# Kernel optimization log

Hardware: AMD Instinct MI355X
Metric: run time of the kernel (lower is better)

The kernel has to match this reference:

```python
import jax, jax.numpy as jnp
import numpy as np

N = 3072      # num topics / nodes
D_IN = 64     # topic_dim
HID = 128     # hidden_dim
NH = 4        # n_heads
HD = HID // NH
L = 2         # n_gat_layers
B = 1024      # batch of topic_ids
ALPHA = 0.2   # leaky relu slope
TD = 0.1      # time decay
EPS = 1e-5    # layernorm eps


def setup_inputs() -> dict:
    key = jax.random.key(0)
    ks = jax.random.split(key, 16)
    rn = lambda k, s, sc=0.05: (jax.random.normal(k, s, jnp.float32) * sc)
    return {
        "topic_ids": jax.random.randint(ks[0], (B,), 0, N, dtype=jnp.int32),
        "adj_matrix": jax.random.randint(ks[1], (N, N), 0, 2).astype(jnp.float32),
        "time_matrix": jax.random.uniform(ks[2], (N, N), dtype=jnp.float32),
        "attractiveness": jax.random.normal(ks[3], (B,), jnp.float32),
        "topic_emb": rn(ks[4], (N, D_IN), 0.1),
        "Ws": rn(ks[5], (D_IN, HID)), "bs": jnp.zeros((HID,), jnp.float32),
        "Wa": rn(ks[6], (1, HID)), "ba": jnp.zeros((HID,), jnp.float32),
        "gat_W": rn(ks[7], (L, NH, HID, HD)),
        "gat_a": rn(ks[8], (L, NH, 2 * HD, 1)),
        "ln_g": jnp.ones((L, HID), jnp.float32),
        "ln_b": jnp.zeros((L, HID), jnp.float32),
        "W1": rn(ks[9], (HID, HID)), "b1": jnp.zeros((HID,), jnp.float32),
        "W2": rn(ks[10], (HID, 1)), "b2": jnp.zeros((1,), jnp.float32),
    }


def _gat_layer(x, adj, tmat, W, a, g, b):
    # x: [1, N, HID], adj/tmat: [N, N], W: [NH, HID, HD], a: [NH, 2*HD, 1]
    time_weights = jnp.exp(-TD * (tmat.max() - tmat))          # [N, N]
    h = jnp.einsum('bni,hio->bhno', x, W)                      # [1, NH, N, HD]
    a_src, a_dst = a[:, :HD, 0], a[:, HD:, 0]                  # [NH, HD]
    e_src = jnp.einsum('bhnd,hd->bhn', h, a_src)               # [1, NH, N]
    e_dst = jnp.einsum('bhnd,hd->bhn', h, a_dst)
    e = e_src[:, :, :, None] + e_dst[:, :, None, :]            # [1, NH, N, N]
    e = jax.nn.leaky_relu(e, ALPHA) * time_weights[None, None]
    mask = adj[None, None]                                     # [1, 1, N, N]
    e = jnp.where(mask == 0, -jnp.inf, e)
    has_nb = mask.sum(axis=-1) > 0                             # [1, 1, N]
    e = jnp.where(has_nb[..., None], e, 0.0)                   # isolated rows -> zeros -> uniform softmax (matches torch)
    att = jax.nn.softmax(e, axis=-1)
    att = jnp.where(jnp.isnan(att), 0.0, att)
    out = jnp.einsum('bhij,bhjo->bhio', att, h)                # [1, NH, N, HD]
    out = out.transpose(0, 2, 1, 3).reshape(1, N, NH * HD)
    out = jax.nn.elu(out)
    mu = out.mean(axis=-1, keepdims=True)
    var = out.var(axis=-1, keepdims=True)
    return (out - mu) / jnp.sqrt(var + EPS) * g + b


def reference(topic_ids, adj_matrix, time_matrix, attractiveness, topic_emb,
              Ws, bs, Wa, ba, gat_W, gat_a, ln_g, ln_b, W1, b1, W2, b2):
    struct = topic_emb @ Ws + bs                               # [N, HID]
    attract = attractiveness[:, None] @ Wa + ba                # [B, HID]
    x = struct[None]                                           # [1, N, HID]
    for l in range(L):
        x = _gat_layer(x, adj_matrix, time_matrix, gat_W[l], gat_a[l], ln_g[l], ln_b[l])
    topic_feats = x[0][topic_ids]                              # [B, HID]
    hidden = jax.nn.relu((topic_feats + attract) @ W1 + b1)
    return hidden @ W2 + b2                                    # [B, 1]
```

## Files before the change

kernel.cpp:

```cpp
#include <hip/hip_runtime.h>
#include <hip/hip_fp16.h>

#define N 3072
#define D_IN 64
#define HID 128
#define NH 4
#define HD 32
#define NB 1024
#define ALPHA 0.2f
#define TD 0.1f
#define EPS 1e-5f
#define LOG2E 1.4426950408889634f
#define TSPLIT 16
#define JSPAN (N / TSPLIT)
#define NCH (JSPAN / 64)
#define PSTR 72

typedef unsigned int uint;
typedef unsigned short ushort;
typedef __attribute__((ext_vector_type(8))) __bf16 bf16x8;
typedef __attribute__((ext_vector_type(4))) float f32x4;

__device__ __forceinline__ ushort f2bf(float f) {
  union { float f; uint u; } c; c.f = f;
  uint u = c.u;
  return (ushort)((u + 0x7FFFu + ((u >> 16) & 1u)) >> 16);
}

__global__ __launch_bounds__(256) void k_prep1(const float4* __restrict__ tmat4,
                                               uint* __restrict__ tmax_u) {
  int g = blockIdx.x * 256 + threadIdx.x;
  float mx = 0.f;
#pragma unroll
  for (int k = 0; k < 9; k++) {
    float4 v = tmat4[g + k * 262144];
    mx = fmaxf(mx, fmaxf(fmaxf(v.x, v.y), fmaxf(v.z, v.w)));
  }
  for (int o = 32; o > 0; o >>= 1) mx = fmaxf(mx, __shfl_xor(mx, o));
  __shared__ float sm[4];
  if ((threadIdx.x & 63) == 0) sm[threadIdx.x >> 6] = mx;
  __syncthreads();
  if (threadIdx.x == 0) {
    float m = fmaxf(fmaxf(sm[0], sm[1]), fmaxf(sm[2], sm[3]));
    atomicMax(tmax_u, __float_as_uint(m));
  }
}

__global__ __launch_bounds__(256) void k_prep2(const float* __restrict__ tmat,
                                               const float* __restrict__ adj,
                                               const uint* __restrict__ tmax_u,
                                               ushort* __restrict__ aw,
                                               uint* __restrict__ deg0) {
  int row = blockIdx.x * 4 + (threadIdx.x >> 6);
  int lane = threadIdx.x & 63;
  float tmax = __uint_as_float(*tmax_u);
  const float c1 = TD * LOG2E;
  const float4* tr = (const float4*)(tmat + (size_t)row * N);
  const float4* ar = (const float4*)(adj + (size_t)row * N);
  ushort* ao = aw + (size_t)row * N;
  float s = 0.f;
#pragma unroll
  for (int it = 0; it < 12; it++) {
    int c4 = lane + it * 64;
    float4 t4 = tr[c4];
    float4 a4 = ar[c4];
    s += a4.x + a4.y + a4.z + a4.w;
    float w0 = __builtin_amdgcn_exp2f(c1 * (t4.x - tmax)) * LOG2E;
    float w1 = __builtin_amdgcn_exp2f(c1 * (t4.y - tmax)) * LOG2E;
    float w2 = __builtin_amdgcn_exp2f(c1 * (t4.z - tmax)) * LOG2E;
    float w3 = __builtin_amdgcn_exp2f(c1 * (t4.w - tmax)) * LOG2E;
    ushort u0 = (a4.x != 0.f) ? __half_as_ushort(__float2half(w0)) : (ushort)0;
    ushort u1 = (a4.y != 0.f) ? __half_as_ushort(__float2half(w1)) : (ushort)0;
    ushort u2 = (a4.z != 0.f) ? __half_as_ushort(__float2half(w2)) : (ushort)0;
    ushort u3 = (a4.w != 0.f) ? __half_as_ushort(__float2half(w3)) : (ushort)0;
    uint2 pk;
    pk.x = (uint)u0 | ((uint)u1 << 16);
    pk.y = (uint)u2 | ((uint)u3 << 16);
    *(uint2*)(ao + c4 * 4) = pk;
  }
  for (int o = 32; o > 0; o >>= 1) s += __shfl_xor(s, o);
  if (lane == 0) deg0[row] = (s == 0.f) ? 1u : 0u;
}

__global__ __launch_bounds__(128) void k_struct(const float* __restrict__ emb,
                                                const float* __restrict__ Ws,
                                                const float* __restrict__ bs,
                                                float* __restrict__ x0) {
  int n = blockIdx.x, c = threadIdx.x;
  __shared__ float es_[D_IN];
  if (c < D_IN) es_[c] = emb[n * D_IN + c];
  __syncthreads();
  float acc = bs[c];
#pragma unroll
  for (int i = 0; i < D_IN; i++) acc += es_[i] * Ws[i * HID + c];
  x0[(size_t)n * HID + c] = acc;
}

__global__ __launch_bounds__(256) void k_h(const float* __restrict__ x,
                                           const float* __restrict__ gW,
                                           const float* __restrict__ gA,
                                           ushort* __restrict__ hT,
                                           float* __restrict__ es,
                                           float* __restrict__ ed) {
  int n0 = blockIdx.x * 8;
  int t = threadIdx.x;
  __shared__ float xs[8][HID];
  __shared__ float hs[8][HID];
  for (int k = t; k < 8 * HID; k += 256) xs[k >> 7][k & 127] = x[(size_t)n0 * HID + k];
  __syncthreads();
  int c = t & 127, rh = t >> 7;
  const float* Wc = gW + (c >> 5) * (HID * HD) + (c & 31);
  float acc[4] = {0.f, 0.f, 0.f, 0.f};
  for (int i = 0; i < HID; i++) {
    float wv = Wc[i * HD];
#pragma unroll
    for (int r4 = 0; r4 < 4; r4++) acc[r4] += xs[rh + 2 * r4][i] * wv;
  }
#pragma unroll
  for (int r4 = 0; r4 < 4; r4++) hs[rh + 2 * r4][c] = acc[r4];
  __syncthreads();
  if (t < 64) {
    int r = t >> 3, h_ = (t >> 1) & 3, sd = t & 1;
    const float* av = gA + h_ * (2 * HD) + sd * HD;
    float d = 0.f;
#pragma unroll
    for (int k = 0; k < HD; k++) d += hs[r][h_ * HD + k] * av[k];
    (sd ? ed : es)[h_ * N + n0 + r] = d;
  }
  {
    int half = t >> 7;
    ushort pk[4];
#pragma unroll
    for (int r = 0; r < 4; r++) pk[r] = f2bf(hs[half * 4 + r][c]);
    uint2 v;
    v.x = (uint)pk[0] | ((uint)pk[1] << 16);
    v.y = (uint)pk[2] | ((uint)pk[3] << 16);
    *(uint2*)(&hT[(size_t)c * N + n0 + half * 4]) = v;
  }
}

__global__ __launch_bounds__(256) void k_att(const ushort* __restrict__ aw,
                                             const ushort* __restrict__ hT,
                                             const float* __restrict__ es,
                                             const float* __restrict__ ed,
                                             const uint* __restrict__ deg0,
                                             float* __restrict__ o_part,
                                             float* __restrict__ s_part) {
  __shared__ __align__(16) ushort ps[2][NH][32][PSTR];
  int tid = threadIdx.x;
  int ib = blockIdx.x * 32;
  int sp = blockIdx.y;
  int jb0 = sp * JSPAN;

  int jl = tid & 31;
  int ig = tid >> 5;
  float esr[4][NH];
  uint dg[4];
#pragma unroll
  for (int p = 0; p < 4; p++) {
    int i = ib + ig + 8 * p;
    dg[p] = deg0[i];
#pragma unroll
    for (int h_ = 0; h_ < NH; h_++) esr[p][h_] = es[h_ * N + i];
  }

  int wv = tid >> 6;
  int ln = tid & 63;
  f32x4 acc00 = {0.f, 0.f, 0.f, 0.f}, acc01 = {0.f, 0.f, 0.f, 0.f};
  f32x4 acc10 = {0.f, 0.f, 0.f, 0.f}, acc11 = {0.f, 0.f, 0.f, 0.f};
  float sacc[4][NH];
#pragma unroll
  for (int p = 0; p < 4; p++)
#pragma unroll
    for (int h_ = 0; h_ < NH; h_++) sacc[p][h_] = 0.f;

  uint awv[4];
  float2 edv[NH];

  auto LOADS = [&](int ch) {
    int j0 = jb0 + ch * 64 + 2 * jl;
#pragma unroll
    for (int p = 0; p < 4; p++)
      awv[p] = *(const uint*)&aw[(size_t)(ib + ig + 8 * p) * N + j0];
#pragma unroll
    for (int h_ = 0; h_ < NH; h_++) edv[h_] = *(const float2*)&ed[h_ * N + j0];
  };
  auto COMPUTE = [&](int buf) {
#pragma unroll
    for (int p = 0; p < 4; p++) {
      float a0 = __half2float(__ushort_as_half((ushort)(awv[p] & 0xFFFFu)));
      float a1 = __half2float(__ushort_as_half((ushort)(awv[p] >> 16)));
#pragma unroll
      for (int h_ = 0; h_ < NH; h_++) {
        float e0 = esr[p][h_] + edv[h_].x;
        float e1 = esr[p][h_] + edv[h_].y;
        float l0 = fmaxf(e0, 0.f) + ALPHA * fminf(e0, 0.f);
        float l1 = fmaxf(e1, 0.f) + ALPHA * fminf(e1, 0.f);
        float p0 = __builtin_amdgcn_exp2f(l0 * a0);
        float p1 = __builtin_amdgcn_exp2f(l1 * a1);
        p0 = (a0 != 0.f) ? p0 : 0.f;
        p1 = (a1 != 0.f) ? p1 : 0.f;
        if (dg[p]) { p0 = 1.f; p1 = 1.f; }
        sacc[p][h_] += p0 + p1;
        uint pk = (__float_as_uint(p0) >> 16) | (__float_as_uint(p1) & 0xFFFF0000u);
        *(uint*)&ps[buf][h_][ig + 8 * p][2 * jl] = pk;
      }
    }
  };

  LOADS(0);
  COMPUTE(0);

  int r = ln & 15, g = ln >> 4;
  for (int ch = 0; ch < NCH; ch++) {
    __syncthreads();
    if (ch + 1 < NCH) LOADS(ch + 1);
    {
      int jb = jb0 + ch * 64;
      const ushort* hTb = hT + (size_t)(wv * HD) * N + jb;
      int buf = ch & 1;
#pragma unroll
      for (int ks = 0; ks < 2; ks++) {
        bf16x8 a0f = *(const bf16x8*)&ps[buf][wv][r][ks * 32 + g * 8];
        bf16x8 a1f = *(const bf16x8*)&ps[buf][wv][16 + r][ks * 32 + g * 8];
        bf16x8 b0 = *(const bf16x8*)(hTb + (size_t)r * N + ks * 32 + g * 8);
        bf16x8 b1 = *(const bf16x8*)(hTb + (size_t)(16 + r) * N + ks * 32 + g * 8);
        acc00 = __builtin_amdgcn_mfma_f32_16x16x32_bf16(a0f, b0, acc00, 0, 0, 0);
        acc01 = __builtin_amdgcn_mfma_f32_16x16x32_bf16(a0f, b1, acc01, 0, 0, 0);
        acc10 = __builtin_amdgcn_mfma_f32_16x16x32_bf16(a1f, b0, acc10, 0, 0, 0);
        acc11 = __builtin_amdgcn_mfma_f32_16x16x32_bf16(a1f, b1, acc11, 0, 0, 0);
      }
    }
    if (ch + 1 < NCH) COMPUTE((ch + 1) & 1);
  }

#pragma unroll
  for (int p = 0; p < 4; p++)
#pragma unroll
    for (int h_ = 0; h_ < NH; h_++) {
      float v = sacc[p][h_];
      v += __shfl_xor(v, 16); v += __shfl_xor(v, 8);
      v += __shfl_xor(v, 4);  v += __shfl_xor(v, 2); v += __shfl_xor(v, 1);
      if (jl == 0) {
        int i = ib + ig + 8 * p;
        s_part[((size_t)sp * N + i) * NH + h_] = v;
      }
    }
  {
#pragma unroll
    for (int q = 0; q < 4; q++) {
      int i0 = ib + g * 4 + q;
      int i1 = ib + 16 + g * 4 + q;
      float* op0 = o_part + ((size_t)sp * N + i0) * HID + wv * HD;
      float* op1 = o_part + ((size_t)sp * N + i1) * HID + wv * HD;
      op0[r] = acc00[q];
      op0[16 + r] = acc01[q];
      op1[r] = acc10[q];
      op1[16 + r] = acc11[q];
    }
  }
}

__global__ __launch_bounds__(128) void k_combine(const float* __restrict__ o_part,
                                                 const float* __restrict__ s_part,
                                                 const float* __restrict__ g,
                                                 const float* __restrict__ b,
                                                 float* __restrict__ xout) {
  int i = blockIdx.x, c = threadIdx.x;
  float o = 0.f, s = 0.f;
#pragma unroll
  for (int sp = 0; sp < TSPLIT; sp++) {
    o += o_part[((size_t)sp * N + i) * HID + c];
    s += s_part[((size_t)sp * N + i) * NH + (c >> 5)];
  }
  float v = o / s;
  v = v > 0.f ? v : expm1f(v);
  float sm = v, sq = v * v;
  for (int off = 32; off > 0; off >>= 1) { sm += __shfl_xor(sm, off); sq += __shfl_xor(sq, off); }
  __shared__ float s2[2][2];
  int w = c >> 6, l = c & 63;
  if (l == 0) { s2[w][0] = sm; s2[w][1] = sq; }
  __syncthreads();
  float tot = s2[0][0] + s2[1][0], totq = s2[0][1] + s2[1][1];
  float mu = tot / (float)HID;
  float var = totq / (float)HID - mu * mu;
  float rs = rsqrtf(var + EPS);
  xout[(size_t)i * HID + c] = (v - mu) * rs * g[c] + b[c];
}

__global__ __launch_bounds__(128) void k_final(const float* __restrict__ x,
                                               const int* __restrict__ tid,
                                               const float* __restrict__ attr,
                                               const float* __restrict__ Wa,
                                               const float* __restrict__ ba,
                                               const float* __restrict__ W1,
                                               const float* __restrict__ b1,
                                               const float* __restrict__ W2,
                                               const float* __restrict__ b2,
                                               float* __restrict__ out) {
  int bI = blockIdx.x, c = threadIdx.x;
  __shared__ float tf[HID];
  __shared__ float red[2];
  int id = tid[bI];
  float av = attr[bI];
  tf[c] = x[(size_t)id * HID + c] + av * Wa[c] + ba[c];
  __syncthreads();
  float acc = b1[c];
  for (int i = 0; i < HID; i++) acc += tf[i] * W1[i * HID + c];
  acc = fmaxf(acc, 0.f);
  float pr = acc * W2[c];
  for (int off = 32; off > 0; off >>= 1) pr += __shfl_xor(pr, off);
  int w = c >> 6, l = c & 63;
  if (l == 0) red[w] = pr;
  __syncthreads();
  if (c == 0) out[bI] = red[0] + red[1] + b2[0];
}

extern "C" void kernel_launch(void* const* d_in, const int* in_sizes, int n_in,
                              void* d_out, int out_size, void* d_ws, size_t ws_size,
                              hipStream_t stream) {
  (void)in_sizes; (void)n_in; (void)out_size; (void)ws_size;
  const int*   topic_ids = (const int*)d_in[0];
  const float* adj  = (const float*)d_in[1];
  const float* tmat = (const float*)d_in[2];
  const float* attr = (const float*)d_in[3];
  const float* emb  = (const float*)d_in[4];
  const float* Ws   = (const float*)d_in[5];
  const float* bs   = (const float*)d_in[6];
  const float* Wa   = (const float*)d_in[7];
  const float* ba   = (const float*)d_in[8];
  const float* gW   = (const float*)d_in[9];
  const float* gA   = (const float*)d_in[10];
  const float* lng  = (const float*)d_in[11];
  const float* lnb  = (const float*)d_in[12];
  const float* W1   = (const float*)d_in[13];
  const float* b1   = (const float*)d_in[14];
  const float* W2   = (const float*)d_in[15];
  const float* b2   = (const float*)d_in[16];

  char* ws = (char*)d_ws;
  size_t o = 0;
  auto alloc = [&](size_t bytes) { void* p = ws + o; o += (bytes + 255) & ~255ull; return p; };
  uint*   tmax_u = (uint*)alloc(4);
  uint*   deg0   = (uint*)alloc((size_t)N * 4);
  float*  X0     = (float*)alloc((size_t)N * HID * 4);
  float*  X1     = (float*)alloc((size_t)N * HID * 4);
  float*  X2     = (float*)alloc((size_t)N * HID * 4);
  ushort* hT     = (ushort*)alloc((size_t)HID * N * 2);
  float*  es     = (float*)alloc((size_t)NH * N * 4);
  float*  ed     = (float*)alloc((size_t)NH * N * 4);
  float*  o_part = (float*)alloc((size_t)TSPLIT * N * HID * 4);
  float*  s_part = (float*)alloc((size_t)TSPLIT * N * NH * 4);
  ushort* aw     = (ushort*)alloc((size_t)N * N * 2);

  hipMemsetAsync(tmax_u, 0, 4, stream);
  k_prep1<<<1024, 256, 0, stream>>>((const float4*)tmat, tmax_u);
  k_prep2<<<N / 4, 256, 0, stream>>>(tmat, adj, tmax_u, aw, deg0);
  k_struct<<<N, 128, 0, stream>>>(emb, Ws, bs, X0);

  const float* xin = X0;
  float* xouts[2] = {X1, X2};
  for (int l = 0; l < 2; l++) {
    k_h<<<N / 8, 256, 0, stream>>>(xin, gW + (size_t)l * NH * HID * HD,
                                   gA + (size_t)l * NH * 2 * HD, hT, es, ed);
    dim3 gr(N / 32, TSPLIT);
    k_att<<<gr, 256, 0, stream>>>(aw, hT, es, ed, deg0, o_part, s_part);
    k_combine<<<N, 128, 0, stream>>>(o_part, s_part, lng + l * HID, lnb + l * HID, xouts[l]);
    xin = xouts[l];
  }
  k_final<<<NB, 128, 0, stream>>>(X2, topic_ids, attr, Wa, ba, W1, b1, W2, b2, (float*)d_out);
}
```

Baseline: 249.0 us.

## Fuse prep, struct and combine kernels; recompute masked time weights inside attention

Merges the time-max and degree passes into one prep kernel. The masked fp16 time-weight matrix is no longer materialised; k_att reads the fp32 time and adjacency matrices directly and recomputes the exp weight per element. The struct projection and the split-softmax combine/ELU/LayerNorm are folded into the h-projection kernel, and the final combine into k_final, which removes the intermediate X buffers and several launches. In exchange, each attention pass reads two fp32 N×N matrices instead of one fp16 matrix, which roughly quadruples its adjacency/time traffic unless it is served from the large last-level cache.

```diff
diff --git a/kernel.cpp b/kernel.cpp
--- a/kernel.cpp
+++ b/kernel.cpp
@@ -1,5 +1,4 @@
 #include <hip/hip_runtime.h>
-#include <hip/hip_fp16.h>
 
 #define N 3072
 #define D_IN 64
@@ -27,87 +26,91 @@
   return (ushort)((u + 0x7FFFu + ((u >> 16) & 1u)) >> 16);
 }
 
-__global__ __launch_bounds__(256) void k_prep1(const float4* __restrict__ tmat4,
-                                               uint* __restrict__ tmax_u) {
-  int g = blockIdx.x * 256 + threadIdx.x;
-  float mx = 0.f;
-#pragma unroll
-  for (int k = 0; k < 9; k++) {
-    float4 v = tmat4[g + k * 262144];
-    mx = fmaxf(mx, fmaxf(fmaxf(v.x, v.y), fmaxf(v.z, v.w)));
-  }
-  for (int o = 32; o > 0; o >>= 1) mx = fmaxf(mx, __shfl_xor(mx, o));
-  __shared__ float sm[4];
-  if ((threadIdx.x & 63) == 0) sm[threadIdx.x >> 6] = mx;
-  __syncthreads();
-  if (threadIdx.x == 0) {
-    float m = fmaxf(fmaxf(sm[0], sm[1]), fmaxf(sm[2], sm[3]));
-    atomicMax(tmax_u, __float_as_uint(m));
-  }
-}
-
-__global__ __launch_bounds__(256) void k_prep2(const float* __restrict__ tmat,
-                                               const float* __restrict__ adj,
-                                               const uint* __restrict__ tmax_u,
-                                               ushort* __restrict__ aw,
-                                               uint* __restrict__ deg0) {
+__global__ __launch_bounds__(256) void k_prep(const float* __restrict__ tmat,
+                                              const float* __restrict__ adj,
+                                              uint* __restrict__ tmax_u,
+                                              uint* __restrict__ deg0) {
   int row = blockIdx.x * 4 + (threadIdx.x >> 6);
   int lane = threadIdx.x & 63;
-  float tmax = __uint_as_float(*tmax_u);
-  const float c1 = TD * LOG2E;
   const float4* tr = (const float4*)(tmat + (size_t)row * N);
   const float4* ar = (const float4*)(adj + (size_t)row * N);
-  ushort* ao = aw + (size_t)row * N;
-  float s = 0.f;
+  float mx = 0.f, s = 0.f;
 #pragma unroll
   for (int it = 0; it < 12; it++) {
-    int c4 = lane + it * 64;
-    float4 t4 = tr[c4];
-    float4 a4 = ar[c4];
+    float4 t4 = tr[lane + it * 64];
+    float4 a4 = ar[lane + it * 64];
+    mx = fmaxf(mx, fmaxf(fmaxf(t4.x, t4.y), fmaxf(t4.z, t4.w)));
     s += a4.x + a4.y + a4.z + a4.w;
-    float w0 = __builtin_amdgcn_exp2f(c1 * (t4.x - tmax)) * LOG2E;
-    float w1 = __builtin_amdgcn_exp2f(c1 * (t4.y - tmax)) * LOG2E;
-    float w2 = __builtin_amdgcn_exp2f(c1 * (t4.z - tmax)) * LOG2E;
-    float w3 = __builtin_amdgcn_exp2f(c1 * (t4.w - tmax)) * LOG2E;
-    ushort u0 = (a4.x != 0.f) ? __half_as_ushort(__float2half(w0)) : (ushort)0;
-    ushort u1 = (a4.y != 0.f) ? __half_as_ushort(__float2half(w1)) : (ushort)0;
-    ushort u2 = (a4.z != 0.f) ? __half_as_ushort(__float2half(w2)) : (ushort)0;
-    ushort u3 = (a4.w != 0.f) ? __half_as_ushort(__float2half(w3)) : (ushort)0;
-    uint2 pk;
-    pk.x = (uint)u0 | ((uint)u1 << 16);
-    pk.y = (uint)u2 | ((uint)u3 << 16);
-    *(uint2*)(ao + c4 * 4) = pk;
-  }
-  for (int o = 32; o > 0; o >>= 1) s += __shfl_xor(s, o);
-  if (lane == 0) deg0[row] = (s == 0.f) ? 1u : 0u;
-}
-
-__global__ __launch_bounds__(128) void k_struct(const float* __restrict__ emb,
-                                                const float* __restrict__ Ws,
-                                                const float* __restrict__ bs,
-                                                float* __restrict__ x0) {
-  int n = blockIdx.x, c = threadIdx.x;
-  __shared__ float es_[D_IN];
-  if (c < D_IN) es_[c] = emb[n * D_IN + c];
-  __syncthreads();
-  float acc = bs[c];
-#pragma unroll
-  for (int i = 0; i < D_IN; i++) acc += es_[i] * Ws[i * HID + c];
-  x0[(size_t)n * HID + c] = acc;
-}
-
-__global__ __launch_bounds__(256) void k_h(const float* __restrict__ x,
-                                           const float* __restrict__ gW,
-                                           const float* __restrict__ gA,
-                                           ushort* __restrict__ hT,
-                                           float* __restrict__ es,
-                                           float* __restrict__ ed) {
+  }
+  for (int o = 32; o > 0; o >>= 1) { mx = fmaxf(mx, __shfl_xor(mx, o)); s += __shfl_xor(s, o); }
+  __shared__ float smx[4];
+  int w = threadIdx.x >> 6;
+  if (lane == 0) { deg0[row] = (s == 0.f) ? 1u : 0u; smx[w] = mx; }
+  __syncthreads();
+  if (threadIdx.x == 0) {
+    float m = fmaxf(fmaxf(smx[0], smx[1]), fmaxf(smx[2], smx[3]));
+    atomicMax(tmax_u, __float_as_uint(m));
+  }
+}
+
+__global__ __launch_bounds__(256) void k_hx(int layer,
+                                            const float* __restrict__ emb,
+                                            const float* __restrict__ Ws,
+                                            const float* __restrict__ bs,
+                                            const float* __restrict__ o_part,
+                                            const float* __restrict__ s_part,
+                                            const float* __restrict__ lg,
+                                            const float* __restrict__ lb,
+                                            const float* __restrict__ gW,
+                                            const float* __restrict__ gA,
+                                            ushort* __restrict__ hT,
+                                            float* __restrict__ es,
+                                            float* __restrict__ ed) {
   int n0 = blockIdx.x * 8;
   int t = threadIdx.x;
   __shared__ float xs[8][HID];
   __shared__ float hs[8][HID];
-  for (int k = t; k < 8 * HID; k += 256) xs[k >> 7][k & 127] = x[(size_t)n0 * HID + k];
-  __syncthreads();
+  __shared__ float embs[8][D_IN];
+
+  if (layer == 0) {
+    for (int k = t; k < 8 * D_IN; k += 256) embs[k >> 6][k & 63] = emb[n0 * D_IN + k];
+    __syncthreads();
+    int c = t & 127, rh = t >> 7;
+#pragma unroll
+    for (int k = 0; k < 4; k++) {
+      int r = rh + 2 * k;
+      float acc = bs[c];
+#pragma unroll
+      for (int i = 0; i < D_IN; i++) acc += embs[r][i] * Ws[i * HID + c];
+      xs[r][c] = acc;
+    }
+  } else {
+    int w = t >> 6, l = t & 63;
+    int h = l >> 4;
+#pragma unroll
+    for (int rr = 0; rr < 2; rr++) {
+      int i = n0 + 2 * w + rr;
+      float ox = 0.f, oy = 0.f, sden = 0.f;
+#pragma unroll
+      for (int sp = 0; sp < TSPLIT; sp++) {
+        float2 ov = *(const float2*)&o_part[((size_t)sp * N + i) * HID + 2 * l];
+        ox += ov.x; oy += ov.y;
+        sden += s_part[((size_t)sp * N + i) * NH + h];
+      }
+      float v0 = ox / sden, v1 = oy / sden;
+      v0 = v0 > 0.f ? v0 : expm1f(v0);
+      v1 = v1 > 0.f ? v1 : expm1f(v1);
+      float sm = v0 + v1, sq = v0 * v0 + v1 * v1;
+      for (int o = 32; o > 0; o >>= 1) { sm += __shfl_xor(sm, o); sq += __shfl_xor(sq, o); }
+      float mu = sm / (float)HID;
+      float var = sq / (float)HID - mu * mu;
+      float rs = rsqrtf(var + EPS);
+      xs[2 * w + rr][2 * l]     = (v0 - mu) * rs * lg[2 * l]     + lb[2 * l];
+      xs[2 * w + rr][2 * l + 1] = (v1 - mu) * rs * lg[2 * l + 1] + lb[2 * l + 1];
+    }
+  }
+  __syncthreads();
+
   int c = t & 127, rh = t >> 7;
   const float* Wc = gW + (c >> 5) * (HID * HD) + (c & 31);
   float acc[4] = {0.f, 0.f, 0.f, 0.f};
@@ -139,7 +142,9 @@
   }
 }
 
-__global__ __launch_bounds__(256) void k_att(const ushort* __restrict__ aw,
+__global__ __launch_bounds__(256) void k_att(const float* __restrict__ tmat,
+                                             const float* __restrict__ adj,
+                                             const uint* __restrict__ tmax_u,
                                              const ushort* __restrict__ hT,
                                              const float* __restrict__ es,
                                              const float* __restrict__ ed,
@@ -151,6 +156,8 @@
   int ib = blockIdx.x * 32;
   int sp = blockIdx.y;
   int jb0 = sp * JSPAN;
+  float tmax = __uint_as_float(*tmax_u);
+  const float c1 = TD * LOG2E;
 
   int jl = tid & 31;
   int ig = tid >> 5;
@@ -174,32 +181,34 @@
 #pragma unroll
     for (int h_ = 0; h_ < NH; h_++) sacc[p][h_] = 0.f;
 
-  uint awv[4];
-  float2 edv[NH];
+  float2 t2v[4], a2v[4], edv[NH];
 
   auto LOADS = [&](int ch) {
     int j0 = jb0 + ch * 64 + 2 * jl;
 #pragma unroll
-    for (int p = 0; p < 4; p++)
-      awv[p] = *(const uint*)&aw[(size_t)(ib + ig + 8 * p) * N + j0];
+    for (int p = 0; p < 4; p++) {
+      t2v[p] = *(const float2*)&tmat[(size_t)(ib + ig + 8 * p) * N + j0];
+      a2v[p] = *(const float2*)&adj[(size_t)(ib + ig + 8 * p) * N + j0];
+    }
 #pragma unroll
     for (int h_ = 0; h_ < NH; h_++) edv[h_] = *(const float2*)&ed[h_ * N + j0];
   };
   auto COMPUTE = [&](int buf) {
 #pragma unroll
     for (int p = 0; p < 4; p++) {
-      float a0 = __half2float(__ushort_as_half((ushort)(awv[p] & 0xFFFFu)));
-      float a1 = __half2float(__ushort_as_half((ushort)(awv[p] >> 16)));
+      float m0 = __builtin_amdgcn_exp2f(c1 * (t2v[p].x - tmax)) * LOG2E;
+      float m1 = __builtin_amdgcn_exp2f(c1 * (t2v[p].y - tmax)) * LOG2E;
+      bool z0 = (a2v[p].x != 0.f), z1 = (a2v[p].y != 0.f);
 #pragma unroll
       for (int h_ = 0; h_ < NH; h_++) {
         float e0 = esr[p][h_] + edv[h_].x;
         float e1 = esr[p][h_] + edv[h_].y;
         float l0 = fmaxf(e0, 0.f) + ALPHA * fminf(e0, 0.f);
         float l1 = fmaxf(e1, 0.f) + ALPHA * fminf(e1, 0.f);
-        float p0 = __builtin_amdgcn_exp2f(l0 * a0);
-        float p1 = __builtin_amdgcn_exp2f(l1 * a1);
-        p0 = (a0 != 0.f) ? p0 : 0.f;
-        p1 = (a1 != 0.f) ? p1 : 0.f;
+        float p0 = __builtin_amdgcn_exp2f(l0 * m0);
+        float p1 = __builtin_amdgcn_exp2f(l1 * m1);
+        p0 = z0 ? p0 : 0.f;
+        p1 = z1 ? p1 : 0.f;
         if (dg[p]) { p0 = 1.f; p1 = 1.f; }
         sacc[p][h_] += p0 + p1;
         uint pk = (__float_as_uint(p0) >> 16) | (__float_as_uint(p1) & 0xFFFF0000u);
@@ -261,34 +270,10 @@
   }
 }
 
-__global__ __launch_bounds__(128) void k_combine(const float* __restrict__ o_part,
-                                                 const float* __restrict__ s_part,
-                                                 const float* __restrict__ g,
-                                                 const float* __restrict__ b,
-                                                 float* __restrict__ xout) {
-  int i = blockIdx.x, c = threadIdx.x;
-  float o = 0.f, s = 0.f;
-#pragma unroll
-  for (int sp = 0; sp < TSPLIT; sp++) {
-    o += o_part[((size_t)sp * N + i) * HID + c];
-    s += s_part[((size_t)sp * N + i) * NH + (c >> 5)];
-  }
-  float v = o / s;
-  v = v > 0.f ? v : expm1f(v);
-  float sm = v, sq = v * v;
-  for (int off = 32; off > 0; off >>= 1) { sm += __shfl_xor(sm, off); sq += __shfl_xor(sq, off); }
-  __shared__ float s2[2][2];
-  int w = c >> 6, l = c & 63;
-  if (l == 0) { s2[w][0] = sm; s2[w][1] = sq; }
-  __syncthreads();
-  float tot = s2[0][0] + s2[1][0], totq = s2[0][1] + s2[1][1];
-  float mu = tot / (float)HID;
-  float var = totq / (float)HID - mu * mu;
-  float rs = rsqrtf(var + EPS);
-  xout[(size_t)i * HID + c] = (v - mu) * rs * g[c] + b[c];
-}
-
-__global__ __launch_bounds__(128) void k_final(const float* __restrict__ x,
+__global__ __launch_bounds__(128) void k_final(const float* __restrict__ o_part,
+                                               const float* __restrict__ s_part,
+                                               const float* __restrict__ lg,
+                                               const float* __restrict__ lb,
                                                const int* __restrict__ tid,
                                                const float* __restrict__ attr,
                                                const float* __restrict__ Wa,
@@ -300,17 +285,35 @@
                                                float* __restrict__ out) {
   int bI = blockIdx.x, c = threadIdx.x;
   __shared__ float tf[HID];
+  __shared__ float s2[2][2];
   __shared__ float red[2];
   int id = tid[bI];
   float av = attr[bI];
-  tf[c] = x[(size_t)id * HID + c] + av * Wa[c] + ba[c];
+  float o = 0.f, sden = 0.f;
+  int h = c >> 5;
+#pragma unroll
+  for (int sp = 0; sp < TSPLIT; sp++) {
+    o += o_part[((size_t)sp * N + id) * HID + c];
+    sden += s_part[((size_t)sp * N + id) * NH + h];
+  }
+  float v = o / sden;
+  v = v > 0.f ? v : expm1f(v);
+  float sm = v, sq = v * v;
+  for (int off = 32; off > 0; off >>= 1) { sm += __shfl_xor(sm, off); sq += __shfl_xor(sq, off); }
+  int w = c >> 6, l = c & 63;
+  if (l == 0) { s2[w][0] = sm; s2[w][1] = sq; }
+  __syncthreads();
+  float tot = s2[0][0] + s2[1][0], totq = s2[0][1] + s2[1][1];
+  float mu = tot / (float)HID;
+  float var = totq / (float)HID - mu * mu;
+  float rs = rsqrtf(var + EPS);
+  tf[c] = (v - mu) * rs * lg[c] + lb[c] + av * Wa[c] + ba[c];
   __syncthreads();
   float acc = b1[c];
   for (int i = 0; i < HID; i++) acc += tf[i] * W1[i * HID + c];
   acc = fmaxf(acc, 0.f);
   float pr = acc * W2[c];
   for (int off = 32; off > 0; off >>= 1) pr += __shfl_xor(pr, off);
-  int w = c >> 6, l = c & 63;
   if (l == 0) red[w] = pr;
   __syncthreads();
   if (c == 0) out[bI] = red[0] + red[1] + b2[0];
@@ -343,30 +346,23 @@
   auto alloc = [&](size_t bytes) { void* p = ws + o; o += (bytes + 255) & ~255ull; return p; };
   uint*   tmax_u = (uint*)alloc(4);
   uint*   deg0   = (uint*)alloc((size_t)N * 4);
-  float*  X0     = (float*)alloc((size_t)N * HID * 4);
-  float*  X1     = (float*)alloc((size_t)N * HID * 4);
-  float*  X2     = (float*)alloc((size_t)N * HID * 4);
   ushort* hT     = (ushort*)alloc((size_t)HID * N * 2);
   float*  es     = (float*)alloc((size_t)NH * N * 4);
   float*  ed     = (float*)alloc((size_t)NH * N * 4);
   float*  o_part = (float*)alloc((size_t)TSPLIT * N * HID * 4);
   float*  s_part = (float*)alloc((size_t)TSPLIT * N * NH * 4);
-  ushort* aw     = (ushort*)alloc((size_t)N * N * 2);
 
   hipMemsetAsync(tmax_u, 0, 4, stream);
-  k_prep1<<<1024, 256, 0, stream>>>((const float4*)tmat, tmax_u);
-  k_prep2<<<N / 4, 256, 0, stream>>>(tmat, adj, tmax_u, aw, deg0);
-  k_struct<<<N, 128, 0, stream>>>(emb, Ws, bs, X0);
-
-  const float* xin = X0;
-  float* xouts[2] = {X1, X2};
-  for (int l = 0; l < 2; l++) {
-    k_h<<<N / 8, 256, 0, stream>>>(xin, gW + (size_t)l * NH * HID * HD,
-                                   gA + (size_t)l * NH * 2 * HD, hT, es, ed);
-    dim3 gr(N / 32, TSPLIT);
-    k_att<<<gr, 256, 0, stream>>>(aw, hT, es, ed, deg0, o_part, s_part);
-    k_combine<<<N, 128, 0, stream>>>(o_part, s_part, lng + l * HID, lnb + l * HID, xouts[l]);
-    xin = xouts[l];
-  }
-  k_final<<<NB, 128, 0, stream>>>(X2, topic_ids, attr, Wa, ba, W1, b1, W2, b2, (float*)d_out);
-}
+  k_prep<<<N / 4, 256, 0, stream>>>(tmat, adj, tmax_u, deg0);
+
+  dim3 gr(N / 32, TSPLIT);
+  k_hx<<<N / 8, 256, 0, stream>>>(0, emb, Ws, bs, nullptr, nullptr, nullptr, nullptr,
+                                  gW, gA, hT, es, ed);
+  k_att<<<gr, 256, 0, stream>>>(tmat, adj, tmax_u, hT, es, ed, deg0, o_part, s_part);
+  k_hx<<<N / 8, 256, 0, stream>>>(1, nullptr, nullptr, nullptr, o_part, s_part, lng, lnb,
+                                  gW + (size_t)NH * HID * HD, gA + (size_t)NH * 2 * HD,
+                                  hT, es, ed);
+  k_att<<<gr, 256, 0, stream>>>(tmat, adj, tmax_u, hT, es, ed, deg0, o_part, s_part);
+  k_final<<<NB, 128, 0, stream>>>(o_part, s_part, lng + HID, lnb + HID,
+                                  topic_ids, attr, Wa, ba, W1, b1, W2, b2, (float*)d_out);
+}
```

Result: slower. 265.3 us (+6.6%).
